# Optimization experiments

Measured on AMD Instinct MI355X. Metric: run time of the kernel, lower is better.

## Reference

```python
import jax, jax.numpy as jnp
import numpy as np
import math

B, N, XD, ED, H = 8, 128, 256, 128, 8
DF = XD // H
FFX, FFE = 1024, 512


def _lin(x, w, b):
    return x @ w + b


def _ln(x, g, b):
    m = x.mean(-1, keepdims=True)
    v = ((x - m) ** 2).mean(-1, keepdims=True)
    return (x - m) / jnp.sqrt(v + 1e-5) * g + b


def setup_inputs() -> dict:
    key = jax.random.key(0)
    ks = jax.random.split(key, 16)
    d = {}
    d['x'] = jax.random.normal(ks[0], (B, N, XD), jnp.float32)
    d['e'] = jax.random.normal(ks[1], (B, N, N, ED), jnp.float32)
    wspecs = [('wq', (XD, XD)), ('wk', (XD, XD)), ('wv', (XD, XD)),
              ('wem', (ED, XD)), ('wea', (ED, XD)), ('wxo', (XD, XD)),
              ('weo', (XD, ED)), ('wx1', (XD, FFX)), ('wx2', (FFX, XD)),
              ('we1', (ED, FFE)), ('we2', (FFE, ED))]
    for i, (name, shp) in enumerate(wspecs):
        d[name] = jax.random.normal(ks[2 + i % 14], shp, jnp.float32) * 0.02
        d[name] = jax.random.normal(jax.random.fold_in(key, i + 10), shp, jnp.float32) * 0.02
    for name, dim in [('bq', XD), ('bk', XD), ('bv', XD), ('bem', XD), ('bea', XD),
                      ('bxo', XD), ('beo', ED), ('bx1', FFX), ('bx2', XD),
                      ('be1', FFE), ('be2', ED)]:
        d[name] = jnp.zeros((dim,), jnp.float32)
    d['gnx'] = jnp.ones((XD,), jnp.float32)
    d['bnx'] = jnp.zeros((XD,), jnp.float32)
    d['gne'] = jnp.ones((ED,), jnp.float32)
    d['bne'] = jnp.zeros((ED,), jnp.float32)
    return d


def reference(x, e, wq, wk, wv, wem, wea, wxo, weo, wx1, wx2, we1, we2,
              bq, bk, bv, bem, bea, bxo, beo, bx1, bx2, be1, be2,
              gnx, bnx, gne, bne):
    # --- NodeEdgeBlock ---
    Q = _lin(x, wq, bq).reshape(B, N, H, DF)
    K = _lin(x, wk, bk).reshape(B, N, H, DF)
    # per-channel outer product: (B, N_i, N_j, H, DF)
    Y = Q[:, :, None] * K[:, None] / math.sqrt(DF)
    E1 = _lin(e, wem, bem).reshape(B, N, N, H, DF)
    E2 = _lin(e, wea, bea).reshape(B, N, N, H, DF)
    Y = Y * (E1 + 1.0) + E2
    newE = _lin(Y.reshape(B, N, N, XD), weo, beo)
    attn = jax.nn.softmax(Y, axis=1)  # softmax over source-node axis i
    V = _lin(x, wv, bv := bv if False else bv).reshape(B, N, H, DF) if False else _lin(x, wv, bv).reshape(B, N, H, DF)
    wV = (attn * V[:, None]).sum(axis=1).reshape(B, N, XD)
    newX = _lin(wV, wxo, bxo)

    # --- FF blocks (dropout=0 => identity); note the SAME norm (norm2) is applied twice,
    # and the second residual uses the pre-norm input, matching the torch code. ---
    def ff(inp, new, w1, b1, w2, b2, g, bn):
        h = _ln(inp + new, g, bn)
        h = jax.nn.relu(_lin(h, w1, b1))
        h = _lin(h, w2, b2)
        return _ln(inp + h, g, bn)

    x_out = ff(x, newX, wx1, bx1, wx2, bx2, gnx, bnx)
    e_out = ff(e, newE, we1, be1, we2, be2, gne, bne)
    return (x_out, e_out)
```

## Files before the change

kernel.cpp:

```cpp
#include <hip/hip_runtime.h>


#define RSQRT_DF 0.17677669529663687f

typedef __attribute__((ext_vector_type(8))) short short8;
typedef __attribute__((ext_vector_type(4))) short short4v;
typedef __attribute__((ext_vector_type(4))) float f32x4;

__device__ __forceinline__ short f2bs(float f) {
    unsigned u = __float_as_uint(f);
    unsigned r = u + 0x7FFFu + ((u >> 16) & 1u);
    return (short)(r >> 16);
}
__device__ __forceinline__ float bs2f(short s) {
    return __uint_as_float(((unsigned)(unsigned short)s) << 16);
}

struct PackArgs {
    const float* W[11];
    short* Wp[11];
    int kdiv[11];
    int N[11];
    int start[12];
};

__global__ __launch_bounds__(256) void pack_all(PackArgs pa) {
    int g = blockIdx.x * 256 + threadIdx.x;
    if (g >= pa.start[11]) return;
    int i = 0;
    while (g >= pa.start[i + 1]) ++i;
    int local = g - pa.start[i];
    int kdiv = pa.kdiv[i], N = pa.N[i];
    int lane = local & 63, rest = local >> 6;
    int kb = rest % kdiv, nt = rest / kdiv;
    int n = nt * 16 + (lane & 15);
    int k0 = kb * 32 + ((lane >> 4) << 3);
    const float* W = pa.W[i];
    short8 v;
#pragma unroll
    for (int j = 0; j < 8; ++j) v[j] = f2bs(W[(size_t)(k0 + j) * N + n]);
    *(short8*)(pa.Wp[i] + (size_t)local * 8) = v;
}

__global__ __launch_bounds__(256) void qk_gemm(
    const float* __restrict__ x,
    const short* __restrict__ wqP, const short* __restrict__ wkP,
    const float* __restrict__ bq, const float* __restrict__ bk,
    float* __restrict__ Qb, float* __restrict__ Kb) {
    __shared__ short sXb[16 * 264];
    const int t = threadIdx.x, wave = t >> 6, lane = t & 63;
    const int quad = lane >> 4, l15 = lane & 15;
    const int m0 = (blockIdx.x & 63) * 16;
    const int isK = blockIdx.x >> 6;
    const short* wP = isK ? wkP : wqP;
    const float* bp = isK ? bk : bq;
    float* outp = isK ? Kb : Qb;

    const float4* x4 = (const float4*)(x + (size_t)m0 * 256);
    for (int g = t; g < 1024; g += 256) {
        float4 v = x4[g];
        int row = g >> 6, col4 = (g & 63) * 4;
        short4v sv = {f2bs(v.x), f2bs(v.y), f2bs(v.z), f2bs(v.w)};
        *(short4v*)(sXb + row * 264 + col4) = sv;
    }
    __syncthreads();

#pragma unroll 2
    for (int p = 0; p < 4; ++p) {
        int nt = wave * 4 + p;
        f32x4 acc = (f32x4){0.f, 0.f, 0.f, 0.f};
        const short* aB = sXb + l15 * 264 + quad * 8;
        const short* bB = wP + ((size_t)(nt * 8) * 64 + lane) * 8;
#pragma unroll
        for (int kb = 0; kb < 8; ++kb) {
            short8 a = *(const short8*)(aB + kb * 32);
            short8 w = *(const short8*)(bB + (size_t)kb * 512);
            acc = __builtin_amdgcn_mfma_f32_16x16x32_bf16(a, w, acc, 0, 0, 0);
        }
        int col = nt * 16 + l15;
        float bvv = bp[col];
#pragma unroll
        for (int r = 0; r < 4; ++r)
            outp[(size_t)(m0 + quad * 4 + r) * 256 + col] = acc[r] + bvv;
    }
}

__global__ __launch_bounds__(512, 3) void fused_main(
    const float* __restrict__ x, const float* __restrict__ e,
    const float* __restrict__ Qb, const float* __restrict__ Kb,
    const short* __restrict__ wvP, const short* __restrict__ wxoP,
    const short* __restrict__ wx1P, const short* __restrict__ wx2P,
    const short* __restrict__ wemP, const short* __restrict__ weaP,
    const short* __restrict__ weoP, const short* __restrict__ we1P,
    const short* __restrict__ we2P,
    const float* __restrict__ bv, const float* __restrict__ bxo,
    const float* __restrict__ bx1, const float* __restrict__ bx2,
    const float* __restrict__ bem, const float* __restrict__ bea,
    const float* __restrict__ beo, const float* __restrict__ be1,
    const float* __restrict__ be2,
    const float* __restrict__ gnx, const float* __restrict__ bnx,
    const float* __restrict__ gne, const float* __restrict__ bne,
    float* __restrict__ xout, float* __restrict__ eout) {
    __shared__ __align__(16) char ldsbuf[68608];
    const int t = threadIdx.x, wave = t >> 6, lane = t & 63;
    const int quad = lane >> 4, l15 = lane & 15;

    if (blockIdx.x < 32) {
        short* sXb  = (short*)ldsbuf;
        short* sVb  = (short*)(ldsbuf + 16896);
        short* sTbx = (short*)(ldsbuf + 33792);
        short* sRx  = (short*)(ldsbuf + 50688);
        short* sH1x = (short*)(ldsbuf + 50688);
        short* sH2x = (short*)(ldsbuf + 50688);
        const int m0 = blockIdx.x * 32;

        const float4* x4 = (const float4*)(x + (size_t)m0 * 256);
        for (int g = t; g < 2048; g += 512) {
            float4 v = x4[g];
            int row = g >> 6, col4 = (g & 63) * 4;
            short4v sv = {f2bs(v.x), f2bs(v.y), f2bs(v.z), f2bs(v.w)};
            *(short4v*)(sXb + row * 264 + col4) = sv;
        }
        __syncthreads();

#pragma unroll
        for (int ctl = 0; ctl < 2; ++ctl) {
            const int ct = wave * 2 + ctl;
            const int c0 = ct * 16 + quad * 4;
            const short* bB = wvP + ((size_t)(ct * 8) * 64 + lane) * 8;
            short8 w[8];
#pragma unroll
            for (int kb = 0; kb < 8; ++kb) w[kb] = *(const short8*)(bB + (size_t)kb * 512);
            const float4 bvv = *(const float4*)(bv + c0);
#pragma unroll
            for (int rt = 0; rt < 2; ++rt) {
                const int row = rt * 16 + l15;
                f32x4 acc = (f32x4){0.f, 0.f, 0.f, 0.f};
#pragma unroll
                for (int kb = 0; kb < 8; ++kb) {
                    short8 bf = *(const short8*)(sXb + row * 264 + quad * 8 + kb * 32);
                    acc = __builtin_amdgcn_mfma_f32_16x16x32_bf16(w[kb], bf, acc, 0, 0, 0);
                }
                short4v vv = {f2bs(acc[0] + bvv.x), f2bs(acc[1] + bvv.y),
                              f2bs(acc[2] + bvv.z), f2bs(acc[3] + bvv.w)};
                *(short4v*)(sVb + row * 264 + c0) = vv;
            }
        }
        __syncthreads();

#pragma unroll
        for (int ctl = 0; ctl < 2; ++ctl) {
            const int ct = wave * 2 + ctl;
            const int c0 = ct * 16 + quad * 4;
            const short* bB = wxoP + ((size_t)(ct * 8) * 64 + lane) * 8;
            short8 w[8];
#pragma unroll
            for (int kb = 0; kb < 8; ++kb) w[kb] = *(const short8*)(bB + (size_t)kb * 512);
            const float4 bvv = *(const float4*)(bxo + c0);
#pragma unroll
            for (int rt = 0; rt < 2; ++rt) {
                const int row = rt * 16 + l15;
                f32x4 acc = (f32x4){0.f, 0.f, 0.f, 0.f};
#pragma unroll
                for (int kb = 0; kb < 8; ++kb) {
                    short8 bf = *(const short8*)(sVb + row * 264 + quad * 8 + kb * 32);
                    acc = __builtin_amdgcn_mfma_f32_16x16x32_bf16(w[kb], bf, acc, 0, 0, 0);
                }
                short4v vv = {f2bs(acc[0] + bvv.x), f2bs(acc[1] + bvv.y),
                              f2bs(acc[2] + bvv.z), f2bs(acc[3] + bvv.w)};
                *(short4v*)(sRx + row * 264 + c0) = vv;
            }
        }
        __syncthreads();

        for (int rr = 0; rr < 4; ++rr) {
            int row = wave * 4 + rr;
            float v[4];
            float s1 = 0.f, s2 = 0.f;
#pragma unroll
            for (int k = 0; k < 4; ++k) {
                v[k] = bs2f(sXb[row * 264 + lane + 64 * k]) + bs2f(sRx[row * 264 + lane + 64 * k]);
                s1 += v[k]; s2 += v[k] * v[k];
            }
            for (int off = 32; off; off >>= 1) {
                s1 += __shfl_down(s1, off);
                s2 += __shfl_down(s2, off);
            }
            s1 = __shfl(s1, 0); s2 = __shfl(s2, 0);
            float mean = s1 * (1.f / 256.f);
            float var = s2 * (1.f / 256.f) - mean * mean;
            float rstd = rsqrtf(var + 1e-5f);
#pragma unroll
            for (int k = 0; k < 4; ++k)
                sTbx[row * 264 + lane + 64 * k] =
                    f2bs((v[k] - mean) * rstd * gnx[lane + 64 * k] + bnx[lane + 64 * k]);
        }
        __syncthreads();

        f32x4 accEx[2][2];
#pragma unroll
        for (int i = 0; i < 2; ++i)
#pragma unroll
            for (int j = 0; j < 2; ++j) accEx[i][j] = (f32x4){0.f, 0.f, 0.f, 0.f};

        for (int q = 0; q < 4; ++q) {
#pragma unroll
            for (int ctl = 0; ctl < 2; ++ctl) {
                const int ctg = q * 16 + wave * 2 + ctl;
                const int c0 = (wave * 2 + ctl) * 16 + quad * 4;
                const short* bB = wx1P + ((size_t)(ctg * 8) * 64 + lane) * 8;
                short8 w[8];
#pragma unroll
                for (int kb = 0; kb < 8; ++kb) w[kb] = *(const short8*)(bB + (size_t)kb * 512);
                const float4 bvv = *(const float4*)(bx1 + ctg * 16 + quad * 4);
#pragma unroll
                for (int rt = 0; rt < 2; ++rt) {
                    const int row = rt * 16 + l15;
                    f32x4 acc = (f32x4){0.f, 0.f, 0.f, 0.f};
#pragma unroll
                    for (int kb = 0; kb < 8; ++kb) {
                        short8 bf = *(const short8*)(sTbx + row * 264 + quad * 8 + kb * 32);
                        acc = __builtin_amdgcn_mfma_f32_16x16x32_bf16(w[kb], bf, acc, 0, 0, 0);
                    }
                    short4v hv = {f2bs(fmaxf(acc[0] + bvv.x, 0.f)), f2bs(fmaxf(acc[1] + bvv.y, 0.f)),
                                  f2bs(fmaxf(acc[2] + bvv.z, 0.f)), f2bs(fmaxf(acc[3] + bvv.w, 0.f))};
                    *(short4v*)(sH1x + row * 264 + c0) = hv;
                }
            }
            __syncthreads();
#pragma unroll
            for (int ctl = 0; ctl < 2; ++ctl) {
                const int ct = wave * 2 + ctl;
                const short* bB = wx2P + ((size_t)(ct * 32 + q * 8) * 64 + lane) * 8;
                short8 w[8];
#pragma unroll
                for (int kb = 0; kb < 8; ++kb) w[kb] = *(const short8*)(bB + (size_t)kb * 512);
#pragma unroll
                for (int rt = 0; rt < 2; ++rt) {
                    const int row = rt * 16 + l15;
#pragma unroll
                    for (int kb = 0; kb < 8; ++kb) {
                        short8 bf = *(const short8*)(sH1x + row * 264 + quad * 8 + kb * 32);
                        accEx[ctl][rt] = __builtin_amdgcn_mfma_f32_16x16x32_bf16(w[kb], bf, accEx[ctl][rt], 0, 0, 0);
                    }
                }
            }
            __syncthreads();
        }
#pragma unroll
        for (int ctl = 0; ctl < 2; ++ctl) {
            const int c0 = (wave * 2 + ctl) * 16 + quad * 4;
            const float4 bvv = *(const float4*)(bx2 + c0);
#pragma unroll
            for (int rt = 0; rt < 2; ++rt) {
                const int row = rt * 16 + l15;
                short4v hv = {f2bs(accEx[ctl][rt][0] + bvv.x), f2bs(accEx[ctl][rt][1] + bvv.y),
                              f2bs(accEx[ctl][rt][2] + bvv.z), f2bs(accEx[ctl][rt][3] + bvv.w)};
                *(short4v*)(sH2x + row * 264 + c0) = hv;
            }
        }
        __syncthreads();

        for (int rr = 0; rr < 4; ++rr) {
            int row = wave * 4 + rr;
            float v[4];
            float s1 = 0.f, s2 = 0.f;
#pragma unroll
            for (int k = 0; k < 4; ++k) {
                v[k] = bs2f(sXb[row * 264 + lane + 64 * k]) + bs2f(sH2x[row * 264 + lane + 64 * k]);
                s1 += v[k]; s2 += v[k] * v[k];
            }
            for (int off = 32; off; off >>= 1) {
                s1 += __shfl_down(s1, off);
                s2 += __shfl_down(s2, off);
            }
            s1 = __shfl(s1, 0); s2 = __shfl(s2, 0);
            float mean = s1 * (1.f / 256.f);
            float var = s2 * (1.f / 256.f) - mean * mean;
            float rstd = rsqrtf(var + 1e-5f);
#pragma unroll
            for (int k = 0; k < 4; ++k)
                xout[(size_t)(m0 + row) * 256 + lane + 64 * k] =
                    (v[k] - mean) * rstd * gnx[lane + 64 * k] + bnx[lane + 64 * k];
        }
        return;
    }

    short* sEb = (short*)ldsbuf;
    short* sYb = (short*)(ldsbuf + 17408);
    short* sTb = (short*)(ldsbuf + 17408);
    float* sH2 = (float*)(ldsbuf + 17408);
    short* sR  = (short*)(ldsbuf + 51200);
    short* sH1 = (short*)(ldsbuf + 51200);

    const int r0 = (blockIdx.x - 32) * 64;
    const int b = r0 >> 14;
    const int j0 = r0 & 127;

    {
        const float4* e4 = (const float4*)(e + (size_t)r0 * 128);
        for (int g = t; g < 2048; g += 512) {
            float4 v = e4[g];
            int row = g >> 5, col4 = (g & 31) * 4;
            short4v sv = {f2bs(v.x), f2bs(v.y), f2bs(v.z), f2bs(v.w)};
            *(short4v*)(sEb + row * 136 + col4) = sv;
        }
    }
    __syncthreads();

#pragma unroll
    for (int ctl = 0; ctl < 2; ++ctl) {
        const int ct = wave * 2 + ctl;
        const int c0 = ct * 16 + quad * 4;
        const short* p1 = wemP + ((size_t)(ct * 4) * 64 + lane) * 8;
        const short* p2 = weaP + ((size_t)(ct * 4) * 64 + lane) * 8;
        short8 w1[4], w2[4];
#pragma unroll
        for (int kb = 0; kb < 4; ++kb) {
            w1[kb] = *(const short8*)(p1 + (size_t)kb * 512);
            w2[kb] = *(const short8*)(p2 + (size_t)kb * 512);
        }
        const float4 qv  = *(const float4*)(Qb + (size_t)(r0 >> 7) * 256 + c0);
        const float4 bmv = *(const float4*)(bem + c0);
        const float4 bav = *(const float4*)(bea + c0);
#pragma unroll
        for (int rt = 0; rt < 4; ++rt) {
            const int row = rt * 16 + l15;
            const float4 kv = *(const float4*)(Kb + (size_t)((b << 7) + j0 + row) * 256 + c0);
            f32x4 a1 = (f32x4){0.f, 0.f, 0.f, 0.f};
            f32x4 a2 = (f32x4){0.f, 0.f, 0.f, 0.f};
#pragma unroll
            for (int kb = 0; kb < 4; ++kb) {
                short8 bf = *(const short8*)(sEb + row * 136 + quad * 8 + kb * 32);
                a1 = __builtin_amdgcn_mfma_f32_16x16x32_bf16(w1[kb], bf, a1, 0, 0, 0);
                a2 = __builtin_amdgcn_mfma_f32_16x16x32_bf16(w2[kb], bf, a2, 0, 0, 0);
            }
            short4v yv = {
                f2bs(qv.x * RSQRT_DF * kv.x * (a1[0] + bmv.x + 1.0f) + (a2[0] + bav.x)),
                f2bs(qv.y * RSQRT_DF * kv.y * (a1[1] + bmv.y + 1.0f) + (a2[1] + bav.y)),
                f2bs(qv.z * RSQRT_DF * kv.z * (a1[2] + bmv.z + 1.0f) + (a2[2] + bav.z)),
                f2bs(qv.w * RSQRT_DF * kv.w * (a1[3] + bmv.w + 1.0f) + (a2[3] + bav.w))};
            *(short4v*)(sYb + row * 264 + c0) = yv;
        }
    }
    __syncthreads();

    {
        const short* pC = weoP + ((size_t)(wave * 8) * 64 + lane) * 8;
        short8 wC[8];
#pragma unroll
        for (int kb = 0; kb < 8; ++kb) wC[kb] = *(const short8*)(pC + (size_t)kb * 512);
        const int c0 = wave * 16 + quad * 4;
        const float4 bov = *(const float4*)(beo + c0);
#pragma unroll
        for (int rt = 0; rt < 4; ++rt) {
            const int row = rt * 16 + l15;
            f32x4 acc = (f32x4){0.f, 0.f, 0.f, 0.f};
#pragma unroll
            for (int kb = 0; kb < 8; ++kb) {
                short8 bf = *(const short8*)(sYb + row * 264 + quad * 8 + kb * 32);
                acc = __builtin_amdgcn_mfma_f32_16x16x32_bf16(wC[kb], bf, acc, 0, 0, 0);
            }
            short4v rv = {f2bs(acc[0] + bov.x), f2bs(acc[1] + bov.y),
                          f2bs(acc[2] + bov.z), f2bs(acc[3] + bov.w)};
            *(short4v*)(sR + row * 136 + c0) = rv;
        }
    }
    __syncthreads();

    {
        float g0 = gne[lane], g1 = gne[lane + 64];
        float bn0 = bne[lane], bn1 = bne[lane + 64];
        for (int rr = 0; rr < 8; ++rr) {
            int row = wave * 8 + rr;
            float v0 = bs2f(sEb[row * 136 + lane]) + bs2f(sR[row * 136 + lane]);
            float v1 = bs2f(sEb[row * 136 + lane + 64]) + bs2f(sR[row * 136 + lane + 64]);
            float s1 = v0 + v1, s2 = v0 * v0 + v1 * v1;
            for (int off = 32; off; off >>= 1) {
                s1 += __shfl_down(s1, off);
                s2 += __shfl_down(s2, off);
            }
            s1 = __shfl(s1, 0); s2 = __shfl(s2, 0);
            float mean = s1 * 0.0078125f;
            float var = s2 * 0.0078125f - mean * mean;
            float rstd = rsqrtf(var + 1e-5f);
            sTb[row * 136 + lane]      = f2bs((v0 - mean) * rstd * g0 + bn0);
            sTb[row * 136 + lane + 64] = f2bs((v1 - mean) * rstd * g1 + bn1);
        }
    }
    __syncthreads();

    f32x4 accE[4];
#pragma unroll
    for (int p = 0; p < 4; ++p) accE[p] = (f32x4){0.f, 0.f, 0.f, 0.f};

    for (int q = 0; q < 4; ++q) {
        {
            const int ctg = q * 8 + wave;
            const short* p1 = we1P + ((size_t)(ctg * 4) * 64 + lane) * 8;
            short8 w[4];
#pragma unroll
            for (int kb = 0; kb < 4; ++kb) w[kb] = *(const short8*)(p1 + (size_t)kb * 512);
            const int c0 = wave * 16 + quad * 4;
            const float4 b1v = *(const float4*)(be1 + ctg * 16 + quad * 4);
#pragma unroll
            for (int rt = 0; rt < 4; ++rt) {
                const int row = rt * 16 + l15;
                f32x4 acc = (f32x4){0.f, 0.f, 0.f, 0.f};
#pragma unroll
                for (int kb = 0; kb < 4; ++kb) {
                    short8 bf = *(const short8*)(sTb + row * 136 + quad * 8 + kb * 32);
                    acc = __builtin_amdgcn_mfma_f32_16x16x32_bf16(w[kb], bf, acc, 0, 0, 0);
                }
                short4v hv = {f2bs(fmaxf(acc[0] + b1v.x, 0.f)), f2bs(fmaxf(acc[1] + b1v.y, 0.f)),
                              f2bs(fmaxf(acc[2] + b1v.z, 0.f)), f2bs(fmaxf(acc[3] + b1v.w, 0.f))};
                *(short4v*)(sH1 + row * 136 + c0) = hv;
            }
        }
        __syncthreads();
        {
            const short* p2 = we2P + ((size_t)(wave * 16 + q * 4) * 64 + lane) * 8;
            short8 w[4];
#pragma unroll
            for (int kb = 0; kb < 4; ++kb) w[kb] = *(const short8*)(p2 + (size_t)kb * 512);
#pragma unroll
            for (int rt = 0; rt < 4; ++rt) {
                const int row = rt * 16 + l15;
#pragma unroll
                for (int kb = 0; kb < 4; ++kb) {
                    short8 bf = *(const short8*)(sH1 + row * 136 + quad * 8 + kb * 32);
                    accE[rt] = __builtin_amdgcn_mfma_f32_16x16x32_bf16(w[kb], bf, accE[rt], 0, 0, 0);
                }
            }
        }
        __syncthreads();
    }
    {
        const int c0 = wave * 16 + quad * 4;
        const float4 b2v = *(const float4*)(be2 + c0);
#pragma unroll
        for (int rt = 0; rt < 4; ++rt) {
            const int row = rt * 16 + l15;
            float4 hv = {accE[rt][0] + b2v.x, accE[rt][1] + b2v.y,
                         accE[rt][2] + b2v.z, accE[rt][3] + b2v.w};
            *(float4*)(sH2 + (size_t)row * 132 + c0) = hv;
        }
    }
    __syncthreads();

    {
        float g0 = gne[lane], g1 = gne[lane + 64];
        float bn0 = bne[lane], bn1 = bne[lane + 64];
        for (int rr = 0; rr < 8; ++rr) {
            int row = wave * 8 + rr;
            float v0 = bs2f(sEb[row * 136 + lane]) + sH2[row * 132 + lane];
            float v1 = bs2f(sEb[row * 136 + lane + 64]) + sH2[row * 132 + lane + 64];
            float s1 = v0 + v1, s2 = v0 * v0 + v1 * v1;
            for (int off = 32; off; off >>= 1) {
                s1 += __shfl_down(s1, off);
                s2 += __shfl_down(s2, off);
            }
            s1 = __shfl(s1, 0); s2 = __shfl(s2, 0);
            float mean = s1 * 0.0078125f;
            float var = s2 * 0.0078125f - mean * mean;
            float rstd = rsqrtf(var + 1e-5f);
            size_t o = (size_t)(r0 + row) * 128;
            eout[o + lane]      = (v0 - mean) * rstd * g0 + bn0;
            eout[o + lane + 64] = (v1 - mean) * rstd * g1 + bn1;
        }
    }
}

extern "C" void kernel_launch(void* const* d_in, const int* in_sizes, int n_in,
                              void* d_out, int out_size, void* d_ws, size_t ws_size,
                              hipStream_t stream) {
    const float* x   = (const float*)d_in[0];
    const float* e   = (const float*)d_in[1];
    const float* wq  = (const float*)d_in[2];
    const float* wk  = (const float*)d_in[3];
    const float* wv  = (const float*)d_in[4];
    const float* wem = (const float*)d_in[5];
    const float* wea = (const float*)d_in[6];
    const float* wxo = (const float*)d_in[7];
    const float* weo = (const float*)d_in[8];
    const float* wx1 = (const float*)d_in[9];
    const float* wx2 = (const float*)d_in[10];
    const float* we1 = (const float*)d_in[11];
    const float* we2 = (const float*)d_in[12];
    const float* bq  = (const float*)d_in[13];
    const float* bk  = (const float*)d_in[14];
    const float* bv  = (const float*)d_in[15];
    const float* bem = (const float*)d_in[16];
    const float* bea = (const float*)d_in[17];
    const float* bxo = (const float*)d_in[18];
    const float* beo = (const float*)d_in[19];
    const float* bx1 = (const float*)d_in[20];
    const float* bx2 = (const float*)d_in[21];
    const float* be1 = (const float*)d_in[22];
    const float* be2 = (const float*)d_in[23];
    const float* gnx = (const float*)d_in[24];
    const float* bnx = (const float*)d_in[25];
    const float* gne = (const float*)d_in[26];
    const float* bne = (const float*)d_in[27];

    float* out = (float*)d_out;

    float* ws = (float*)d_ws;
    float* Qb = ws;
    float* Kb = Qb + 262144;
    short* base = (short*)(Kb + 262144);
    short* wqP  = base;
    short* wkP  = wqP + 65536;
    short* wvP  = wkP + 65536;
    short* wxoP = wvP + 65536;
    short* wx1P = wxoP + 65536;
    short* wx2P = wx1P + 262144;
    short* wemP = wx2P + 262144;
    short* weaP = wemP + 32768;
    short* weoP = weaP + 32768;
    short* we1P = weoP + 32768;
    short* we2P = we1P + 65536;

    PackArgs pa;
    const float* Ws[11] = {wq, wk, wv, wxo, wx1, wx2, wem, wea, weo, we1, we2};
    short* Wps[11] = {wqP, wkP, wvP, wxoP, wx1P, wx2P, wemP, weaP, weoP, we1P, we2P};
    int Ks[11] = {256, 256, 256, 256, 256, 1024, 128, 128, 256, 128, 512};
    int Ns[11] = {256, 256, 256, 256, 1024, 256, 256, 256, 128, 512, 128};
    int acc = 0;
    for (int i = 0; i < 11; ++i) {
        pa.W[i] = Ws[i];
        pa.Wp[i] = Wps[i];
        pa.kdiv[i] = Ks[i] >> 5;
        pa.N[i] = Ns[i];
        pa.start[i] = acc;
        acc += (Ns[i] >> 4) * (Ks[i] >> 5) * 64;
    }
    pa.start[11] = acc;
    pack_all<<<(acc + 255) / 256, 256, 0, stream>>>(pa);

    qk_gemm<<<128, 256, 0, stream>>>(x, wqP, wkP, bq, bk, Qb, Kb);

    fused_main<<<2080, 512, 0, stream>>>(
        x, e, Qb, Kb, wvP, wxoP, wx1P, wx2P, wemP, weaP, weoP, we1P, we2P,
        bv, bxo, bx1, bx2, bem, bea, beo, be1, be2,
        gnx, bnx, gne, bne, out, out + 262144);
}
```

Before: 290.8 us.

## Retile edge-path GEMMs into 2x4 wave grid with register-cached LDS operands

Reassigns the eight waves in the edge branch from a column-only split (each wave covering all 64 rows) to a 2-row-half by 4-column-group grid. Each wave loads its 32-row B-operand fragments from LDS into registers once and reuses them across several weight column tiles. This applies to the E1/E2 projection, the weo projection and both FFN GEMMs. The aim is fewer redundant LDS reads per MFMA, at the cost of more registers (fragment arrays plus more weight tiles per wave) and more global weight loads per wave.

```diff
diff --git a/kernel.cpp b/kernel.cpp
--- a/kernel.cpp
+++ b/kernel.cpp
@@ -296,6 +296,8 @@
     const int r0 = (blockIdx.x - 32) * 64;
     const int b = r0 >> 14;
     const int j0 = r0 & 127;
+    const int rhalf = wave >> 2, wq4 = wave & 3;
+    const int rbase = rhalf * 32 + l15;
 
     {
         const float4* e4 = (const float4*)(e + (size_t)r0 * 128);
@@ -308,62 +310,77 @@
     }
     __syncthreads();
 
-#pragma unroll
-    for (int ctl = 0; ctl < 2; ++ctl) {
-        const int ct = wave * 2 + ctl;
-        const int c0 = ct * 16 + quad * 4;
-        const short* p1 = wemP + ((size_t)(ct * 4) * 64 + lane) * 8;
-        const short* p2 = weaP + ((size_t)(ct * 4) * 64 + lane) * 8;
-        short8 w1[4], w2[4];
-#pragma unroll
-        for (int kb = 0; kb < 4; ++kb) {
-            w1[kb] = *(const short8*)(p1 + (size_t)kb * 512);
-            w2[kb] = *(const short8*)(p2 + (size_t)kb * 512);
-        }
-        const float4 qv  = *(const float4*)(Qb + (size_t)(r0 >> 7) * 256 + c0);
-        const float4 bmv = *(const float4*)(bem + c0);
-        const float4 bav = *(const float4*)(bea + c0);
-#pragma unroll
-        for (int rt = 0; rt < 4; ++rt) {
-            const int row = rt * 16 + l15;
-            const float4 kv = *(const float4*)(Kb + (size_t)((b << 7) + j0 + row) * 256 + c0);
-            f32x4 a1 = (f32x4){0.f, 0.f, 0.f, 0.f};
-            f32x4 a2 = (f32x4){0.f, 0.f, 0.f, 0.f};
+    {
+        short8 rf[2][4];
+#pragma unroll
+        for (int rtl = 0; rtl < 2; ++rtl)
+#pragma unroll
+            for (int kb = 0; kb < 4; ++kb)
+                rf[rtl][kb] = *(const short8*)(sEb + (rbase + rtl * 16) * 136 + quad * 8 + kb * 32);
+#pragma unroll
+        for (int ctl = 0; ctl < 4; ++ctl) {
+            const int ct = wq4 * 4 + ctl;
+            const int c0 = ct * 16 + quad * 4;
+            const short* p1 = wemP + ((size_t)(ct * 4) * 64 + lane) * 8;
+            const short* p2 = weaP + ((size_t)(ct * 4) * 64 + lane) * 8;
+            short8 w1[4], w2[4];
 #pragma unroll
             for (int kb = 0; kb < 4; ++kb) {
-                short8 bf = *(const short8*)(sEb + row * 136 + quad * 8 + kb * 32);
-                a1 = __builtin_amdgcn_mfma_f32_16x16x32_bf16(w1[kb], bf, a1, 0, 0, 0);
-                a2 = __builtin_amdgcn_mfma_f32_16x16x32_bf16(w2[kb], bf, a2, 0, 0, 0);
-            }
-            short4v yv = {
-                f2bs(qv.x * RSQRT_DF * kv.x * (a1[0] + bmv.x + 1.0f) + (a2[0] + bav.x)),
-                f2bs(qv.y * RSQRT_DF * kv.y * (a1[1] + bmv.y + 1.0f) + (a2[1] + bav.y)),
-                f2bs(qv.z * RSQRT_DF * kv.z * (a1[2] + bmv.z + 1.0f) + (a2[2] + bav.z)),
-                f2bs(qv.w * RSQRT_DF * kv.w * (a1[3] + bmv.w + 1.0f) + (a2[3] + bav.w))};
-            *(short4v*)(sYb + row * 264 + c0) = yv;
+                w1[kb] = *(const short8*)(p1 + (size_t)kb * 512);
+                w2[kb] = *(const short8*)(p2 + (size_t)kb * 512);
+            }
+            const float4 qv  = *(const float4*)(Qb + (size_t)(r0 >> 7) * 256 + c0);
+            const float4 bmv = *(const float4*)(bem + c0);
+            const float4 bav = *(const float4*)(bea + c0);
+#pragma unroll
+            for (int rtl = 0; rtl < 2; ++rtl) {
+                const int row = rbase + rtl * 16;
+                const float4 kv = *(const float4*)(Kb + (size_t)((b << 7) + j0 + row) * 256 + c0);
+                f32x4 a1 = (f32x4){0.f, 0.f, 0.f, 0.f};
+                f32x4 a2 = (f32x4){0.f, 0.f, 0.f, 0.f};
+#pragma unroll
+                for (int kb = 0; kb < 4; ++kb) {
+                    a1 = __builtin_amdgcn_mfma_f32_16x16x32_bf16(w1[kb], rf[rtl][kb], a1, 0, 0, 0);
+                    a2 = __builtin_amdgcn_mfma_f32_16x16x32_bf16(w2[kb], rf[rtl][kb], a2, 0, 0, 0);
+                }
+                short4v yv = {
+                    f2bs(qv.x * RSQRT_DF * kv.x * (a1[0] + bmv.x + 1.0f) + (a2[0] + bav.x)),
+                    f2bs(qv.y * RSQRT_DF * kv.y * (a1[1] + bmv.y + 1.0f) + (a2[1] + bav.y)),
+                    f2bs(qv.z * RSQRT_DF * kv.z * (a1[2] + bmv.z + 1.0f) + (a2[2] + bav.z)),
+                    f2bs(qv.w * RSQRT_DF * kv.w * (a1[3] + bmv.w + 1.0f) + (a2[3] + bav.w))};
+                *(short4v*)(sYb + row * 264 + c0) = yv;
+            }
         }
     }
     __syncthreads();
 
     {
-        const short* pC = weoP + ((size_t)(wave * 8) * 64 + lane) * 8;
-        short8 wC[8];
-#pragma unroll
-        for (int kb = 0; kb < 8; ++kb) wC[kb] = *(const short8*)(pC + (size_t)kb * 512);
-        const int c0 = wave * 16 + quad * 4;
-        const float4 bov = *(const float4*)(beo + c0);
-#pragma unroll
-        for (int rt = 0; rt < 4; ++rt) {
-            const int row = rt * 16 + l15;
-            f32x4 acc = (f32x4){0.f, 0.f, 0.f, 0.f};
-#pragma unroll
-            for (int kb = 0; kb < 8; ++kb) {
-                short8 bf = *(const short8*)(sYb + row * 264 + quad * 8 + kb * 32);
-                acc = __builtin_amdgcn_mfma_f32_16x16x32_bf16(wC[kb], bf, acc, 0, 0, 0);
-            }
-            short4v rv = {f2bs(acc[0] + bov.x), f2bs(acc[1] + bov.y),
-                          f2bs(acc[2] + bov.z), f2bs(acc[3] + bov.w)};
-            *(short4v*)(sR + row * 136 + c0) = rv;
+        short8 rfY[2][8];
+#pragma unroll
+        for (int rtl = 0; rtl < 2; ++rtl)
+#pragma unroll
+            for (int kb = 0; kb < 8; ++kb)
+                rfY[rtl][kb] = *(const short8*)(sYb + (rbase + rtl * 16) * 264 + quad * 8 + kb * 32);
+#pragma unroll
+        for (int ctl = 0; ctl < 2; ++ctl) {
+            const int ct = wq4 * 2 + ctl;
+            const int c0 = ct * 16 + quad * 4;
+            const short* pC = weoP + ((size_t)(ct * 8) * 64 + lane) * 8;
+            short8 wC[8];
+#pragma unroll
+            for (int kb = 0; kb < 8; ++kb) wC[kb] = *(const short8*)(pC + (size_t)kb * 512);
+            const float4 bov = *(const float4*)(beo + c0);
+#pragma unroll
+            for (int rtl = 0; rtl < 2; ++rtl) {
+                const int row = rbase + rtl * 16;
+                f32x4 acc = (f32x4){0.f, 0.f, 0.f, 0.f};
+#pragma unroll
+                for (int kb = 0; kb < 8; ++kb)
+                    acc = __builtin_amdgcn_mfma_f32_16x16x32_bf16(wC[kb], rfY[rtl][kb], acc, 0, 0, 0);
+                short4v rv = {f2bs(acc[0] + bov.x), f2bs(acc[1] + bov.y),
+                              f2bs(acc[2] + bov.z), f2bs(acc[3] + bov.w)};
+                *(short4v*)(sR + row * 136 + c0) = rv;
+            }
         }
     }
     __syncthreads();
@@ -390,59 +407,77 @@
     }
     __syncthreads();
 
-    f32x4 accE[4];
-#pragma unroll
-    for (int p = 0; p < 4; ++p) accE[p] = (f32x4){0.f, 0.f, 0.f, 0.f};
+    f32x4 accE[2][2];
+#pragma unroll
+    for (int i = 0; i < 2; ++i)
+#pragma unroll
+        for (int j = 0; j < 2; ++j) accE[i][j] = (f32x4){0.f, 0.f, 0.f, 0.f};
 
     for (int q = 0; q < 4; ++q) {
         {
-            const int ctg = q * 8 + wave;
-            const short* p1 = we1P + ((size_t)(ctg * 4) * 64 + lane) * 8;
-            short8 w[4];
-#pragma unroll
-            for (int kb = 0; kb < 4; ++kb) w[kb] = *(const short8*)(p1 + (size_t)kb * 512);
-            const int c0 = wave * 16 + quad * 4;
-            const float4 b1v = *(const float4*)(be1 + ctg * 16 + quad * 4);
-#pragma unroll
-            for (int rt = 0; rt < 4; ++rt) {
-                const int row = rt * 16 + l15;
-                f32x4 acc = (f32x4){0.f, 0.f, 0.f, 0.f};
-#pragma unroll
-                for (int kb = 0; kb < 4; ++kb) {
-                    short8 bf = *(const short8*)(sTb + row * 136 + quad * 8 + kb * 32);
-                    acc = __builtin_amdgcn_mfma_f32_16x16x32_bf16(w[kb], bf, acc, 0, 0, 0);
-                }
-                short4v hv = {f2bs(fmaxf(acc[0] + b1v.x, 0.f)), f2bs(fmaxf(acc[1] + b1v.y, 0.f)),
-                              f2bs(fmaxf(acc[2] + b1v.z, 0.f)), f2bs(fmaxf(acc[3] + b1v.w, 0.f))};
-                *(short4v*)(sH1 + row * 136 + c0) = hv;
+            short8 rfT[2][4];
+#pragma unroll
+            for (int rtl = 0; rtl < 2; ++rtl)
+#pragma unroll
+                for (int kb = 0; kb < 4; ++kb)
+                    rfT[rtl][kb] = *(const short8*)(sTb + (rbase + rtl * 16) * 136 + quad * 8 + kb * 32);
+#pragma unroll
+            for (int ctl = 0; ctl < 2; ++ctl) {
+                const int ctg = q * 8 + wq4 * 2 + ctl;
+                const int c0l = (wq4 * 2 + ctl) * 16 + quad * 4;
+                const short* p1 = we1P + ((size_t)(ctg * 4) * 64 + lane) * 8;
+                short8 w[4];
+#pragma unroll
+                for (int kb = 0; kb < 4; ++kb) w[kb] = *(const short8*)(p1 + (size_t)kb * 512);
+                const float4 b1v = *(const float4*)(be1 + ctg * 16 + quad * 4);
+#pragma unroll
+                for (int rtl = 0; rtl < 2; ++rtl) {
+                    const int row = rbase + rtl * 16;
+                    f32x4 acc = (f32x4){0.f, 0.f, 0.f, 0.f};
+#pragma unroll
+                    for (int kb = 0; kb < 4; ++kb)
+                        acc = __builtin_amdgcn_mfma_f32_16x16x32_bf16(w[kb], rfT[rtl][kb], acc, 0, 0, 0);
+                    short4v hv = {f2bs(fmaxf(acc[0] + b1v.x, 0.f)), f2bs(fmaxf(acc[1] + b1v.y, 0.f)),
+                                  f2bs(fmaxf(acc[2] + b1v.z, 0.f)), f2bs(fmaxf(acc[3] + b1v.w, 0.f))};
+                    *(short4v*)(sH1 + row * 136 + c0l) = hv;
+                }
             }
         }
         __syncthreads();
         {
-            const short* p2 = we2P + ((size_t)(wave * 16 + q * 4) * 64 + lane) * 8;
-            short8 w[4];
-#pragma unroll
-            for (int kb = 0; kb < 4; ++kb) w[kb] = *(const short8*)(p2 + (size_t)kb * 512);
-#pragma unroll
-            for (int rt = 0; rt < 4; ++rt) {
-                const int row = rt * 16 + l15;
-#pragma unroll
-                for (int kb = 0; kb < 4; ++kb) {
-                    short8 bf = *(const short8*)(sH1 + row * 136 + quad * 8 + kb * 32);
-                    accE[rt] = __builtin_amdgcn_mfma_f32_16x16x32_bf16(w[kb], bf, accE[rt], 0, 0, 0);
-                }
-            }
-        }
-        __syncthreads();
-    }
-    {
-        const int c0 = wave * 16 + quad * 4;
+            short8 rfH[2][4];
+#pragma unroll
+            for (int rtl = 0; rtl < 2; ++rtl)
+#pragma unroll
+                for (int kb = 0; kb < 4; ++kb)
+                    rfH[rtl][kb] = *(const short8*)(sH1 + (rbase + rtl * 16) * 136 + quad * 8 + kb * 32);
+#pragma unroll
+            for (int ctl = 0; ctl < 2; ++ctl) {
+                const int ct = wq4 * 2 + ctl;
+                const short* p2 = we2P + ((size_t)(ct * 16 + q * 4) * 64 + lane) * 8;
+                short8 w[4];
+#pragma unroll
+                for (int kb = 0; kb < 4; ++kb) w[kb] = *(const short8*)(p2 + (size_t)kb * 512);
+#pragma unroll
+                for (int rtl = 0; rtl < 2; ++rtl) {
+#pragma unroll
+                    for (int kb = 0; kb < 4; ++kb)
+                        accE[ctl][rtl] = __builtin_amdgcn_mfma_f32_16x16x32_bf16(
+                            w[kb], rfH[rtl][kb], accE[ctl][rtl], 0, 0, 0);
+                }
+            }
+        }
+        __syncthreads();
+    }
+#pragma unroll
+    for (int ctl = 0; ctl < 2; ++ctl) {
+        const int c0 = (wq4 * 2 + ctl) * 16 + quad * 4;
         const float4 b2v = *(const float4*)(be2 + c0);
 #pragma unroll
-        for (int rt = 0; rt < 4; ++rt) {
-            const int row = rt * 16 + l15;
-            float4 hv = {accE[rt][0] + b2v.x, accE[rt][1] + b2v.y,
-                         accE[rt][2] + b2v.z, accE[rt][3] + b2v.w};
+        for (int rtl = 0; rtl < 2; ++rtl) {
+            const int row = rbase + rtl * 16;
+            float4 hv = {accE[ctl][rtl][0] + b2v.x, accE[ctl][rtl][1] + b2v.y,
+                         accE[ctl][rtl][2] + b2v.z, accE[ctl][rtl][3] + b2v.w};
             *(float4*)(sH2 + (size_t)row * 132 + c0) = hv;
         }
     }
```

After: 302.8 us. 4.1% more time.
